# Kernel optimization log

Hardware: AMD Instinct MI355X
Metric: run time of the kernel (lower is better)

Reference implementation:

```python
import jax, jax.numpy as jnp
import numpy as np

N, K, D, C, H = 200000, 256, 12, 9, 32
EPS = 1e-8


def setup_inputs() -> dict:
    key = jax.random.key(0)
    ks = jax.random.split(key, 8)
    probe_pos = jax.random.uniform(ks[0], (N, 3), dtype=jnp.float32)
    mu = jax.random.uniform(ks[1], (K, 3), dtype=jnp.float32)
    log_s = jax.random.normal(ks[2], (K, 3), dtype=jnp.float32) * 0.3 - 1.5
    # quaternions near identity (w~1) as in the torch init
    q = jax.random.normal(ks[3], (K, 4), dtype=jnp.float32) * 0.1 + jnp.array([1.0, 0.0, 0.0, 0.0], jnp.float32)
    F = jax.random.normal(ks[4], (K, D), dtype=jnp.float32) * 0.1
    W1 = jax.random.normal(ks[5], (D + 3, H), dtype=jnp.float32) / np.sqrt(D + 3).astype(np.float32)
    b1 = jnp.zeros((H,), jnp.float32)
    W2 = jax.random.normal(ks[6], (H, C), dtype=jnp.float32) / np.sqrt(H).astype(np.float32)
    b2 = jnp.zeros((C,), jnp.float32)
    return {"probe_pos": probe_pos, "mu": mu, "log_s": log_s, "q": q,
            "F": F, "W1": W1, "b1": b1, "W2": W2, "b2": b2}


def quaternion_to_rotation_matrix(q):
    # q: [K,4] (w,x,y,z) -> [K,3,3]
    q = q / (jnp.linalg.norm(q, axis=-1, keepdims=True) + EPS)
    w, x, y, z = q[..., 0], q[..., 1], q[..., 2], q[..., 3]
    r0 = jnp.stack([1 - 2 * y * y - 2 * z * z, 2 * x * y - 2 * w * z, 2 * x * z + 2 * w * y], axis=-1)
    r1 = jnp.stack([2 * x * y + 2 * w * z, 1 - 2 * x * x - 2 * z * z, 2 * y * z - 2 * w * x], axis=-1)
    r2 = jnp.stack([2 * x * z - 2 * w * y, 2 * y * z + 2 * w * x, 1 - 2 * x * x - 2 * y * y], axis=-1)
    return jnp.stack([r0, r1, r2], axis=-2)


def reference(probe_pos, mu, log_s, q, F, W1, b1, W2, b2):
    s = jnp.exp(log_s)                                   # [K,3]
    R = quaternion_to_rotation_matrix(q)                 # [K,3,3]
    s_inv_sq = 1.0 / (s ** 2 + EPS)                      # [K,3]
    # precision = R @ diag(s_inv_sq) @ R^T -> [K,3,3]
    precision = jnp.einsum('kij,kj,klj->kil', R, s_inv_sq, R)
    diff = probe_pos[:, None, :] - mu[None, :, :]        # [N,K,3]
    mahal = jnp.einsum('nki,kij,nkj->nk', diff, precision, diff)  # [N,K]
    gvals = jnp.exp(-0.5 * mahal)                        # [N,K]
    radii = 3.0 * s.max(axis=1)                          # [K]
    dist = jnp.linalg.norm(diff, axis=2)                 # [N,K]
    gvals = gvals * (dist < radii[None, :]).astype(gvals.dtype)
    weights = gvals / (gvals.sum(axis=1, keepdims=True) + EPS)    # [N,K]
    latent = weights @ F                                 # [N,D]
    mlp_in = jnp.concatenate([latent, probe_pos], axis=1)         # [N,D+3]
    h = jax.nn.relu(mlp_in @ W1 + b1)                    # [N,H]
    sh = h @ W2 + b2                                     # [N,C]
    return (sh, latent, weights)
```

## Files before the change

### kernel.cpp

```cpp
#include <hip/hip_runtime.h>

#define KG 256
#define DD 12
#define HH 32
#define CC 9
#define TPB 256
#define PPB 64
#define KSPL 4
#define KPT 64
#define PSTR 16

typedef float f32x2 __attribute__((ext_vector_type(2)));

__global__ __launch_bounds__(256) void gp_pre(
    const float* __restrict__ mu, const float* __restrict__ log_s,
    const float* __restrict__ q, const float* __restrict__ F,
    float* __restrict__ Ct) {
  int k = threadIdx.x;
  if (k >= KG) return;
  float qw = q[k*4+0], qx = q[k*4+1], qy = q[k*4+2], qz = q[k*4+3];
  float nrm = sqrtf(qw*qw + qx*qx + qy*qy + qz*qz);
  float isn = 1.0f / (nrm + 1e-8f);
  qw *= isn; qx *= isn; qy *= isn; qz *= isn;
  float R00 = 1.f - 2.f*(qy*qy + qz*qz);
  float R01 = 2.f*(qx*qy - qw*qz);
  float R02 = 2.f*(qx*qz + qw*qy);
  float R10 = 2.f*(qx*qy + qw*qz);
  float R11 = 1.f - 2.f*(qx*qx + qz*qz);
  float R12 = 2.f*(qy*qz - qw*qx);
  float R20 = 2.f*(qx*qz - qw*qy);
  float R21 = 2.f*(qy*qz + qw*qx);
  float R22 = 1.f - 2.f*(qx*qx + qy*qy);
  float s0 = expf(log_s[k*3+0]);
  float s1 = expf(log_s[k*3+1]);
  float s2 = expf(log_s[k*3+2]);
  float si0 = 1.f/(s0*s0 + 1e-8f);
  float si1 = 1.f/(s1*s1 + 1e-8f);
  float si2 = 1.f/(s2*s2 + 1e-8f);
  float P00 = R00*si0*R00 + R01*si1*R01 + R02*si2*R02;
  float P01 = R00*si0*R10 + R01*si1*R11 + R02*si2*R12;
  float P02 = R00*si0*R20 + R01*si1*R21 + R02*si2*R22;
  float P11 = R10*si0*R10 + R11*si1*R11 + R12*si2*R12;
  float P12 = R10*si0*R20 + R11*si1*R21 + R12*si2*R22;
  float P22 = R20*si0*R20 + R21*si1*R21 + R22*si2*R22;
  float m0 = mu[k*3+0], m1 = mu[k*3+1], m2 = mu[k*3+2];
  float b0 = P00*m0 + P01*m1 + P02*m2;
  float b1v = P01*m0 + P11*m1 + P12*m2;
  float b2v = P02*m0 + P12*m1 + P22*m2;
  float cterm = m0*b0 + m1*b1v + m2*b2v;
  const float f = -0.7213475204444817f;
  float* c = Ct + k*32;
  c[0] = f*P00;  c[1] = f*P11;  c[2] = f*P22;
  c[3] = 2.f*f*P01;  c[4] = 2.f*f*P02;  c[5] = 2.f*f*P12;
  c[6] = -2.f*f*b0;  c[7] = -2.f*f*b1v; c[8] = -2.f*f*b2v;
  c[9] = f*cterm;
  c[10] = -2.f*m0;  c[11] = -2.f*m1;  c[12] = -2.f*m2;
  c[13] = m0*m0 + m1*m1 + m2*m2;
  float smax = fmaxf(s0, fmaxf(s1, s2));
  c[14] = (3.f*smax)*(3.f*smax);
  c[15] = 0.f;
  #pragma unroll
  for (int d = 0; d < DD; ++d) c[16+d] = F[k*DD + d];
  c[28] = c[29] = c[30] = c[31] = 0.f;
}

__device__ __forceinline__ float gauss_eval(
    const float* __restrict__ c,
    float xx, float yy, float zz, float xy, float xz, float yz,
    float x, float y, float z, float pp) {
  float tp = fmaf(c[0], xx, c[9]);
  tp = fmaf(c[1], yy, tp);
  tp = fmaf(c[2], zz, tp);
  tp = fmaf(c[3], xy, tp);
  tp = fmaf(c[4], xz, tp);
  tp = fmaf(c[5], yz, tp);
  tp = fmaf(c[6], x, tp);
  tp = fmaf(c[7], y, tp);
  tp = fmaf(c[8], z, tp);
  float d2 = pp + c[13];
  d2 = fmaf(c[10], x, d2);
  d2 = fmaf(c[11], y, d2);
  d2 = fmaf(c[12], z, d2);
  float e = __builtin_amdgcn_exp2f(tp);
  return (d2 < c[14]) ? e : 0.0f;
}

__global__ __launch_bounds__(TPB, 7) void gp_main(
    const float* __restrict__ pos, const float* __restrict__ Ct,
    const float* __restrict__ W1, const float* __restrict__ b1,
    const float* __restrict__ W2, const float* __restrict__ b2,
    float* __restrict__ sh_out, float* __restrict__ lat_out,
    float* __restrict__ w_out, int N) {
  __shared__ float part[KSPL * PPB * PSTR];
  __shared__ float4 pxyzi[PPB];
  const int tid  = threadIdx.x;
  const int lane = tid & 63;
  const int wv   = tid >> 6;
  const int pbase = blockIdx.x * PPB;

  if (tid < PPB) {
    int p = pbase + tid; if (p >= N) p = N - 1;
    pxyzi[tid] = make_float4(pos[p*3+0], pos[p*3+1], pos[p*3+2], 0.f);
  }
  __syncthreads();

  const float4 pv = pxyzi[lane];
  const float x = pv.x, y = pv.y, z = pv.z;
  const float xx = x*x, yy = y*y, zz = z*z;
  const float xy = x*y, xz = x*z, yz = y*z;
  const float pp = xx + yy + zz;

  const int kg = __builtin_amdgcn_readfirstlane(wv);
  const float* cbase = Ct + (size_t)(kg * KPT) * 32;
  f32x2 lat2[6];
  #pragma unroll
  for (int j = 0; j < 6; ++j) lat2[j] = (f32x2){0.f, 0.f};
  float dsum = 0.0f;
  #pragma unroll 4
  for (int i = 0; i < KPT; ++i) {
    const float* c = cbase + (i << 5);
    float g = gauss_eval(c, xx, yy, zz, xy, xz, yz, x, y, z, pp);
    dsum += g;
    const f32x2 g2 = (f32x2){g, g};
    const f32x2* f2 = (const f32x2*)(c + 16);
    #pragma unroll
    for (int j = 0; j < 6; ++j)
      lat2[j] = __builtin_elementwise_fma(g2, f2[j], lat2[j]);
  }
  {
    float* pw = part + (wv * PPB + lane) * PSTR;
    *(float4*)(pw + 0) = make_float4(lat2[0].x, lat2[0].y, lat2[1].x, lat2[1].y);
    *(float4*)(pw + 4) = make_float4(lat2[2].x, lat2[2].y, lat2[3].x, lat2[3].y);
    *(float4*)(pw + 8) = make_float4(lat2[4].x, lat2[4].y, lat2[5].x, lat2[5].y);
    *(float4*)(pw +12) = make_float4(dsum, 0.f, 0.f, 0.f);
  }
  __syncthreads();

  float cb[16];
  {
    const float4* r = (const float4*)(Ct + ((size_t)tid << 5));
    *(float4*)&cb[0]  = r[0];
    *(float4*)&cb[4]  = r[1];
    *(float4*)&cb[8]  = r[2];
    *(float4*)&cb[12] = r[3];
  }

  #pragma unroll
  for (int s = tid; s < PPB*13; s += TPB) {
    const int pr = s / 13, j = s - pr*13;
    float a = part[(0*PPB + pr)*PSTR + j] + part[(1*PPB + pr)*PSTR + j]
            + part[(2*PPB + pr)*PSTR + j] + part[(3*PPB + pr)*PSTR + j];
    if (j == 12) pxyzi[pr].w = 1.0f / (a + 1e-8f);
    else part[pr*PSTR + j] = a;
  }
  __syncthreads();

  if (tid < PPB*3) {
    const int pr = tid / 3, q = tid - pr*3;
    if (pbase + pr < N) {
      const float iv = pxyzi[pr].w;
      const float* r = part + pr*PSTR + q*4;
      *(float4*)(lat_out + (size_t)pbase*DD + tid*4) =
          make_float4(r[0]*iv, r[1]*iv, r[2]*iv, r[3]*iv);
    }
  }

  if (tid < PPB && pbase + tid < N) {
    const float inv = pxyzi[tid].w;
    float in15[15];
    #pragma unroll
    for (int j = 0; j < DD; ++j) in15[j] = part[tid*PSTR + j] * inv;
    in15[12] = x; in15[13] = y; in15[14] = z;
    float o[CC];
    #pragma unroll
    for (int c2 = 0; c2 < CC; ++c2) o[c2] = b2[c2];
    #pragma unroll 2
    for (int j = 0; j < HH; ++j) {
      float a = b1[j];
      #pragma unroll
      for (int i = 0; i < 15; ++i) a = fmaf(in15[i], W1[i*HH + j], a);
      a = fmaxf(a, 0.f);
      #pragma unroll
      for (int c2 = 0; c2 < CC; ++c2) o[c2] = fmaf(a, W2[j*CC + c2], o[c2]);
    }
    float* so = sh_out + (size_t)(pbase + tid) * CC;
    #pragma unroll
    for (int c2 = 0; c2 < CC; ++c2) so[c2] = o[c2];
  }

  #pragma unroll 4
  for (int pi = 0; pi < PPB; ++pi) {
    const int lp = (pi + (wv << 4)) & (PPB - 1);
    const float4 b = pxyzi[lp];
    const float bx = b.x, by = b.y, bz = b.z, binv = b.w;
    const float bxx = bx*bx, byy = by*by, bzz = bz*bz;
    const float bxy = bx*by, bxz = bx*bz, byz = by*bz;
    const float bpp = bxx + byy + bzz;
    const float wval = gauss_eval(cb, bxx, byy, bzz, bxy, bxz, byz,
                                  bx, by, bz, bpp) * binv;
    const int gp2 = pbase + lp;
    if (gp2 < N) w_out[(size_t)gp2 * KG + tid] = wval;
  }
}

extern "C" void kernel_launch(void* const* d_in, const int* in_sizes, int n_in,
                              void* d_out, int out_size, void* d_ws, size_t ws_size,
                              hipStream_t stream) {
  const float* probe_pos = (const float*)d_in[0];
  const float* mu        = (const float*)d_in[1];
  const float* log_s     = (const float*)d_in[2];
  const float* q         = (const float*)d_in[3];
  const float* F         = (const float*)d_in[4];
  const float* W1        = (const float*)d_in[5];
  const float* b1        = (const float*)d_in[6];
  const float* W2        = (const float*)d_in[7];
  const float* b2        = (const float*)d_in[8];
  const int N = in_sizes[0] / 3;

  float* Ct = (float*)d_ws;
  float* sh_out  = (float*)d_out;
  float* lat_out = sh_out + (size_t)N*CC;
  float* w_out   = lat_out + (size_t)N*DD;

  gp_pre<<<1, 256, 0, stream>>>(mu, log_s, q, F, Ct);
  const int nb = (N + PPB - 1) / PPB;
  gp_main<<<nb, TPB, 0, stream>>>(probe_pos, Ct, W1, b1, W2, b2,
                                  sh_out, lat_out, w_out, N);
}
```

Baseline: 290.5 us.

## Cache gaussian values in LDS instead of recomputing them for weight output

Each gaussian value computed in the latent accumulation loop is now stored into a 64KB shared-memory tile with XOR swizzling. The weight-output phase reads these values back and scales them by the inverse sum, instead of re-evaluating every gaussian per (point, k). The partial-sum buffer drops its padding to 13 floats, and the launch-bounds occupancy hint goes from 7 to 2 blocks. This removes the redundant second pass of exp and quadratic-form arithmetic, but the large LDS footprint limits resident blocks per CU and reduces latency hiding.

```diff
diff --git a/kernel.cpp b/kernel.cpp
--- a/kernel.cpp
+++ b/kernel.cpp
@@ -8,7 +8,6 @@
 #define PPB 64
 #define KSPL 4
 #define KPT 64
-#define PSTR 16
 
 typedef float f32x2 __attribute__((ext_vector_type(2)));
 
@@ -85,14 +84,16 @@
   return (d2 < c[14]) ? e : 0.0f;
 }
 
-__global__ __launch_bounds__(TPB, 7) void gp_main(
+__global__ __launch_bounds__(TPB, 2) void gp_main(
     const float* __restrict__ pos, const float* __restrict__ Ct,
     const float* __restrict__ W1, const float* __restrict__ b1,
     const float* __restrict__ W2, const float* __restrict__ b2,
     float* __restrict__ sh_out, float* __restrict__ lat_out,
     float* __restrict__ w_out, int N) {
-  __shared__ float part[KSPL * PPB * PSTR];
-  __shared__ float4 pxyzi[PPB];
+  __shared__ float gsh[KG * PPB];
+  __shared__ float part[KSPL * PPB * 13];
+  __shared__ float invL[PPB];
+  __shared__ float4 pxyz[PPB];
   const int tid  = threadIdx.x;
   const int lane = tid & 63;
   const int wv   = tid >> 6;
@@ -100,11 +101,11 @@
 
   if (tid < PPB) {
     int p = pbase + tid; if (p >= N) p = N - 1;
-    pxyzi[tid] = make_float4(pos[p*3+0], pos[p*3+1], pos[p*3+2], 0.f);
+    pxyz[tid] = make_float4(pos[p*3+0], pos[p*3+1], pos[p*3+2], 0.f);
   }
   __syncthreads();
 
-  const float4 pv = pxyzi[lane];
+  const float4 pv = pxyz[lane];
   const float x = pv.x, y = pv.y, z = pv.z;
   const float xx = x*x, yy = y*y, zz = z*z;
   const float xy = x*y, xz = x*z, yz = y*z;
@@ -126,50 +127,43 @@
     #pragma unroll
     for (int j = 0; j < 6; ++j)
       lat2[j] = __builtin_elementwise_fma(g2, f2[j], lat2[j]);
+    const int k = kg * KPT + i;
+    gsh[(k << 6) | (lane ^ (i & 31))] = g;
   }
   {
-    float* pw = part + (wv * PPB + lane) * PSTR;
-    *(float4*)(pw + 0) = make_float4(lat2[0].x, lat2[0].y, lat2[1].x, lat2[1].y);
-    *(float4*)(pw + 4) = make_float4(lat2[2].x, lat2[2].y, lat2[3].x, lat2[3].y);
-    *(float4*)(pw + 8) = make_float4(lat2[4].x, lat2[4].y, lat2[5].x, lat2[5].y);
-    *(float4*)(pw +12) = make_float4(dsum, 0.f, 0.f, 0.f);
+    float* pw = part + (wv * PPB + lane) * 13;
+    pw[0] = lat2[0].x; pw[1] = lat2[0].y; pw[2]  = lat2[1].x; pw[3]  = lat2[1].y;
+    pw[4] = lat2[2].x; pw[5] = lat2[2].y; pw[6]  = lat2[3].x; pw[7]  = lat2[3].y;
+    pw[8] = lat2[4].x; pw[9] = lat2[4].y; pw[10] = lat2[5].x; pw[11] = lat2[5].y;
+    pw[12] = dsum;
   }
   __syncthreads();
-
-  float cb[16];
-  {
-    const float4* r = (const float4*)(Ct + ((size_t)tid << 5));
-    *(float4*)&cb[0]  = r[0];
-    *(float4*)&cb[4]  = r[1];
-    *(float4*)&cb[8]  = r[2];
-    *(float4*)&cb[12] = r[3];
-  }
 
   #pragma unroll
   for (int s = tid; s < PPB*13; s += TPB) {
     const int pr = s / 13, j = s - pr*13;
-    float a = part[(0*PPB + pr)*PSTR + j] + part[(1*PPB + pr)*PSTR + j]
-            + part[(2*PPB + pr)*PSTR + j] + part[(3*PPB + pr)*PSTR + j];
-    if (j == 12) pxyzi[pr].w = 1.0f / (a + 1e-8f);
-    else part[pr*PSTR + j] = a;
+    float a = part[(0*PPB + pr)*13 + j] + part[(1*PPB + pr)*13 + j]
+            + part[(2*PPB + pr)*13 + j] + part[(3*PPB + pr)*13 + j];
+    if (j == 12) invL[pr] = 1.0f / (a + 1e-8f);
+    else part[pr*13 + j] = a;
   }
   __syncthreads();
 
   if (tid < PPB*3) {
     const int pr = tid / 3, q = tid - pr*3;
     if (pbase + pr < N) {
-      const float iv = pxyzi[pr].w;
-      const float* r = part + pr*PSTR + q*4;
+      const float iv = invL[pr];
+      const float* r = part + pr*13 + q*4;
       *(float4*)(lat_out + (size_t)pbase*DD + tid*4) =
           make_float4(r[0]*iv, r[1]*iv, r[2]*iv, r[3]*iv);
     }
   }
 
   if (tid < PPB && pbase + tid < N) {
-    const float inv = pxyzi[tid].w;
+    const float inv = invL[tid];
     float in15[15];
     #pragma unroll
-    for (int j = 0; j < DD; ++j) in15[j] = part[tid*PSTR + j] * inv;
+    for (int j = 0; j < DD; ++j) in15[j] = part[tid*13 + j] * inv;
     in15[12] = x; in15[13] = y; in15[14] = z;
     float o[CC];
     #pragma unroll
@@ -188,18 +182,17 @@
     for (int c2 = 0; c2 < CC; ++c2) so[c2] = o[c2];
   }
 
-  #pragma unroll 4
-  for (int pi = 0; pi < PPB; ++pi) {
-    const int lp = (pi + (wv << 4)) & (PPB - 1);
-    const float4 b = pxyzi[lp];
-    const float bx = b.x, by = b.y, bz = b.z, binv = b.w;
-    const float bxx = bx*bx, byy = by*by, bzz = bz*bz;
-    const float bxy = bx*by, bxz = bx*bz, byz = by*bz;
-    const float bpp = bxx + byy + bzz;
-    const float wval = gauss_eval(cb, bxx, byy, bzz, bxy, bxz, byz,
-                                  bx, by, bz, bpp) * binv;
-    const int gp2 = pbase + lp;
-    if (gp2 < N) w_out[(size_t)gp2 * KG + tid] = wval;
+  {
+    const int kk = tid;
+    const int kb = (kk << 6);
+    const int ks = kk & 31;
+    #pragma unroll 8
+    for (int p = 0; p < PPB; ++p) {
+      const float g  = gsh[kb | (p ^ ks)];
+      const float iv = invL[p];
+      if (pbase + p < N)
+        w_out[(size_t)(pbase + p) * KG + kk] = g * iv;
+    }
   }
 }
 
```

Result: slower. 475.7 us (+63.8%).
